# Kernel tuning notes

Measured on AMD Instinct MI355X. Metric: run time of the kernel, lower is better.

The kernel has to match this reference:

```python
import jax, jax.numpy as jnp
import numpy as np

# Hyperparameters from __init__
TEMPERATURE = 0.07
HARD_POS_W = 1.5
HARD_NEG_W = 2.0
THR_POS = 0.5
THR_NEG = 0.3
NEG_LOSS_W = 0.3

B, D, N_CLASSES = 8192, 256, 1024


def setup_inputs() -> dict:
    key = jax.random.key(0)
    kf, kl = jax.random.split(key)
    features = jax.random.normal(kf, (B, D), dtype=jnp.float32)
    labels = jax.random.randint(kl, (B,), 0, N_CLASSES, dtype=jnp.int32)
    return {"features": features, "labels": labels}


def reference(features, labels):
    b = features.shape[0]
    # L2-normalize features (F.normalize(dim=1))
    anchor = features / jnp.linalg.norm(features, axis=1, keepdims=True)
    sim = anchor @ anchor.T                      # [B, B] cosine similarity
    logits = sim / TEMPERATURE
    logits = logits - jax.lax.stop_gradient(jnp.max(logits, axis=1, keepdims=True))

    mask = (labels[:, None] == labels[None, :]).astype(logits.dtype)   # same-class
    logits_mask = 1.0 - jnp.eye(b, dtype=logits.dtype)                 # exclude self

    # W2ML weights: computed from detached similarities (torch used .item())
    sim_d = jax.lax.stop_gradient(sim)
    offdiag = logits_mask > 0
    is_pos = mask > 0
    hard_pos = is_pos & (sim_d < THR_POS) & offdiag
    pos_weights = jnp.where(
        hard_pos, 1.0 + (THR_POS - sim_d) / THR_POS * (HARD_POS_W - 1.0), 1.0)
    hard_neg = (~is_pos) & (sim_d > THR_NEG) & offdiag
    neg_weights = jnp.where(
        hard_neg, 1.0 + (sim_d - THR_NEG) / (1.0 - THR_NEG) * (HARD_NEG_W - 1.0), 1.0)

    # SupCon log-prob with self excluded from the denominator
    exp_logits = jnp.exp(logits) * logits_mask
    denom = jnp.sum(exp_logits, axis=1, keepdims=True)
    log_prob = logits - jnp.log(denom)

    pos_mask = mask * logits_mask
    pos_cnt = jnp.clip(jnp.sum(pos_mask, axis=1), 1.0, None)
    positive_loss = -jnp.mean(
        jnp.sum(pos_mask * pos_weights * log_prob, axis=1) / pos_cnt)

    # Negative term: weighted mean probability mass assigned to negatives
    neg_mask = (1.0 - mask) * logits_mask
    neg_cnt = jnp.clip(jnp.sum(neg_mask, axis=1), 1.0, None)
    prob = exp_logits / denom
    negative_loss = jnp.mean(
        jnp.sum(neg_mask * neg_weights * prob, axis=1) / neg_cnt)

    return positive_loss + NEG_LOSS_W * negative_loss
```

## Files before the change

kernel.cpp:

```cpp
#include <hip/hip_runtime.h>

#define BSZ  8192
#define DDIM 256
#define BM 128
#define BN 128
#define NT   64
#define NTRI (NT * (NT + 1) / 2)

typedef float f32x4 __attribute__((ext_vector_type(4)));
typedef short bf16x8 __attribute__((ext_vector_type(8)));

__device__ __forceinline__ unsigned short f32_to_bf16(float f) {
    unsigned int u = __float_as_uint(f);
    u += 0x7fffu + ((u >> 16) & 1u);
    return (unsigned short)(u >> 16);
}

#if __has_builtin(__builtin_amdgcn_exp2f)
__device__ __forceinline__ float fast_exp2(float x) { return __builtin_amdgcn_exp2f(x); }
#else
__device__ __forceinline__ float fast_exp2(float x) {
    float r;
    asm("v_exp_f32 %0, %1" : "=v"(r) : "v"(x));
    return r;
}
#endif

#define K_E1   20.60992915555662f
#define K_E2  -20.60992915555662f
#define K_INVT 14.285714285714286f
#define K_N1   1.4285714285714286f
#define K_N2   0.5714285714285714f

template<int CTRL>
__device__ __forceinline__ float dpp_add(float v) {
    int t = __builtin_amdgcn_update_dpp(0, __float_as_int(v), CTRL, 0xF, 0xF, true);
    return v + __int_as_float(t);
}
__device__ __forceinline__ float red16(float v) {
    v = dpp_add<0xB1>(v);
    v = dpp_add<0x4E>(v);
    v = dpp_add<0x141>(v);
    v = dpp_add<0x140>(v);
    return v;
}

__device__ __forceinline__ int swz(int b) {
    return b ^ ((((b >> 7) ^ (b >> 10)) & 7) << 4);
}

__device__ __forceinline__ void decode_tile(int t, int& It, int& Jt) {
    const int off1 = 136, off2 = 392, off3 = 648, off4 = 904, off5 = 1040,
              off6 = 1296, off7 = 1552, off8 = 1688, off9 = 1944;
    int b = (t >= off1) + (t >= off2) + (t >= off3) + (t >= off4) + (t >= off5)
          + (t >= off6) + (t >= off7) + (t >= off8) + (t >= off9);
    int si, sj, r0;
    switch (b) {
        case 0: si = 0; sj = 0; r0 = 0;    break;
        case 1: si = 0; sj = 1; r0 = off1; break;
        case 2: si = 0; sj = 2; r0 = off2; break;
        case 3: si = 0; sj = 3; r0 = off3; break;
        case 4: si = 1; sj = 1; r0 = off4; break;
        case 5: si = 1; sj = 2; r0 = off5; break;
        case 6: si = 1; sj = 3; r0 = off6; break;
        case 7: si = 2; sj = 2; r0 = off7; break;
        case 8: si = 2; sj = 3; r0 = off8; break;
        default: si = 3; sj = 3; r0 = off9; break;
    }
    const int rr = t - r0;
    int il, jl;
    if (si == sj) {
        il = 0;
        #pragma unroll
        for (int q = 1; q < 16; q++) if (rr >= (16 * q - (q * (q - 1)) / 2)) il = q;
        jl = il + (rr - (16 * il - (il * (il - 1)) / 2));
    } else {
        il = rr >> 4;
        jl = rr & 15;
    }
    It = si * 16 + il;
    Jt = sj * 16 + jl;
}

__global__ __launch_bounds__(256) void norm_kernel(const float* __restrict__ feat,
                                                   unsigned short* __restrict__ anchorT,
                                                   float* __restrict__ posAcc,
                                                   unsigned int* __restrict__ counter) {
    __shared__ __align__(16) unsigned short img[8 * 512];
    char* const imgb = (char*)img;
    const int tid  = threadIdx.x;
    const int wid  = tid >> 6;
    const int lane = tid & 63;
    const int R    = blockIdx.x;
    const int R0   = R * 16;

    if (tid < 64) posAcc[blockIdx.x * 64 + tid] = 0.0f;
    if (blockIdx.x == 0 && tid == 0) *counter = 0u;

    #pragma unroll
    for (int it = 0; it < 4; it++) {
        const int row = R0 + it * 4 + wid;
        const float4 v = ((const float4*)(feat + (size_t)row * DDIM))[lane];
        float ss = v.x * v.x + v.y * v.y + v.z * v.z + v.w * v.w;
        #pragma unroll
        for (int off = 32; off > 0; off >>= 1) ss += __shfl_xor(ss, off, 64);
        const float inv = rsqrtf(ss);
        ushort4 o;
        o.x = f32_to_bf16(v.x * inv);
        o.y = f32_to_bf16(v.y * inv);
        o.z = f32_to_bf16(v.z * inv);
        o.w = f32_to_bf16(v.w * inv);
        const int C    = lane >> 3;
        const int l16  = (row & 15) + (((lane >> 1) & 3) << 4);
        const int wb   = (C << 10) + (l16 << 4) + ((lane & 1) << 3);
        *(ushort4*)(imgb + swz(wb)) = o;
    }
    __syncthreads();
    #pragma unroll
    for (int p = 0; p < 2; p++) {
        const int c = p * 4 + wid;
        *(bf16x8*)(anchorT + ((size_t)(c * 512 + R)) * 512 + lane * 8) =
            *(const bf16x8*)(imgb + swz((c << 10) + (lane << 4)));
    }
}

__device__ __forceinline__ void gload_lds16(const unsigned short* g, unsigned short* l) {
    __builtin_amdgcn_global_load_lds(
        (const __attribute__((address_space(1))) void*)g,
        (__attribute__((address_space(3))) void*)l, 16, 0, 0);
}

__global__ __launch_bounds__(512) void simloss_kernel(
    const unsigned short* __restrict__ anchorT,
    const int* __restrict__ labels,
    float* __restrict__ part,
    float* __restrict__ posAcc)
{
    __shared__ __align__(16) unsigned short As[8 * 512];
    __shared__ __align__(16) unsigned short As2[8 * 512];
    __shared__ __align__(16) unsigned short Bs[8 * 512];
    __shared__ __align__(16) unsigned short Bs2[8 * 512];
    __shared__ float rowDT[2][BM][2];
    __shared__ float colDT[4][BN][2];
    __shared__ int rowLab[BM];
    __shared__ int colLab[BN];

    int It, Jt;
    decode_tile(blockIdx.x, It, Jt);
    const bool diag = (It == Jt);
    const int I0 = It * BM, J0 = Jt * BN;

    const int tid  = threadIdx.x;
    const int lane = tid & 63;
    const int w    = tid >> 6;
    const int rw   = w >> 1;
    const int cw   = w & 1;
    const int cl   = lane & 15;
    const int rg   = lane >> 4;
    const int laneOff = lane * 8;

    if (tid < BM) rowLab[tid] = labels[I0 + tid];
    else if (tid < 2 * BM) colLab[tid - BM] = labels[J0 + tid - BM];

    f32x4 acc[2][4];
    #pragma unroll
    for (int f = 0; f < 2; f++)
        #pragma unroll
        for (int g = 0; g < 4; g++)
            acc[f][g] = (f32x4){0.f, 0.f, 0.f, 0.f};

    const unsigned short* aSrc = anchorT + (size_t)It * 4096 + tid * 8;
    const unsigned short* bSrc = anchorT + (size_t)Jt * 4096 + tid * 8;
    unsigned short* const aD0 = &As[w * 512];
    unsigned short* const aD1 = &As2[w * 512];
    unsigned short* const bD0 = &Bs[w * 512];
    unsigned short* const bD1 = &Bs2[w * 512];

    gload_lds16(aSrc, aD0);
    gload_lds16(bSrc, bD0);

    #pragma unroll
    for (int c = 0; c < 8; c++) {
        if (c < 7) {
            const size_t off = (size_t)(c + 1) * 262144;
            gload_lds16(aSrc + off, ((c + 1) & 1) ? aD1 : aD0);
            gload_lds16(bSrc + off, ((c + 1) & 1) ? bD1 : bD0);
            asm volatile("s_waitcnt vmcnt(2)" ::: "memory");
        } else {
            asm volatile("s_waitcnt vmcnt(0)" ::: "memory");
        }
        __builtin_amdgcn_s_barrier();
        __builtin_amdgcn_sched_barrier(0);

        const unsigned short* aB = ((c & 1) ? As2 : As) + (rw * 2) * 512 + laneOff;
        const unsigned short* bB = ((c & 1) ? Bs2 : Bs) + (cw * 4) * 512 + laneOff;
        const bf16x8 a0 = *(const bf16x8*)(aB);
        const bf16x8 a1 = *(const bf16x8*)(aB + 512);
        const bf16x8 b0 = *(const bf16x8*)(bB);
        const bf16x8 b1 = *(const bf16x8*)(bB + 512);
        const bf16x8 b2 = *(const bf16x8*)(bB + 1024);
        const bf16x8 b3 = *(const bf16x8*)(bB + 1536);
        acc[0][0] = __builtin_amdgcn_mfma_f32_16x16x32_bf16(a0, b0, acc[0][0], 0, 0, 0);
        acc[0][1] = __builtin_amdgcn_mfma_f32_16x16x32_bf16(a0, b1, acc[0][1], 0, 0, 0);
        acc[0][2] = __builtin_amdgcn_mfma_f32_16x16x32_bf16(a0, b2, acc[0][2], 0, 0, 0);
        acc[0][3] = __builtin_amdgcn_mfma_f32_16x16x32_bf16(a0, b3, acc[0][3], 0, 0, 0);
        acc[1][0] = __builtin_amdgcn_mfma_f32_16x16x32_bf16(a1, b0, acc[1][0], 0, 0, 0);
        acc[1][1] = __builtin_amdgcn_mfma_f32_16x16x32_bf16(a1, b1, acc[1][1], 0, 0, 0);
        acc[1][2] = __builtin_amdgcn_mfma_f32_16x16x32_bf16(a1, b2, acc[1][2], 0, 0, 0);
        acc[1][3] = __builtin_amdgcn_mfma_f32_16x16x32_bf16(a1, b3, acc[1][3], 0, 0, 0);

        if (c < 7) {
            asm volatile("s_waitcnt lgkmcnt(0)" ::: "memory");
            __builtin_amdgcn_s_barrier();
        }
    }

    int ljr[4], gjr[4];
    #pragma unroll
    for (int g = 0; g < 4; g++) {
        const int cidx = cw * 64 + g * 16 + cl;
        ljr[g] = colLab[cidx];
        gjr[g] = J0 + cidx;
    }
    float cd[4] = {0.f, 0.f, 0.f, 0.f}, ct[4] = {0.f, 0.f, 0.f, 0.f};

    #pragma unroll
    for (int f = 0; f < 2; f++) {
        float rd[4] = {0.f, 0.f, 0.f, 0.f}, rt[4] = {0.f, 0.f, 0.f, 0.f};
        int li[4], gi[4];
        #pragma unroll
        for (int r = 0; r < 4; r++) {
            const int ridx = rw * 32 + f * 16 + rg * 4 + r;
            li[r] = rowLab[ridx];
            gi[r] = I0 + ridx;
        }
        #pragma unroll
        for (int g = 0; g < 4; g++) {
            const int lj = ljr[g];
            const bool granule = (rw * 2 + f) == (cw * 4 + g);
            const f32x4 c = acc[f][g];
            #pragma unroll
            for (int r = 0; r < 4; r++) {
                const float s = c[r];
                const bool self = diag && granule && ((rg * 4 + r) == cl);
                const float e  = self ? 0.f : fast_exp2(fmaf(s, K_E1, K_E2));
                const float wn = fmaxf(fmaf(s, K_N1, K_N2), 1.0f);
                const float we = wn * e;
                rd[r] += e;  rt[r] += we;
                if (!diag) { cd[g] += e; ct[g] += we; }
                if (li[r] == lj && !self) {
                    const float wp = fmaxf(1.5f - s, 1.0f);
                    const float slp = fmaf(s, K_INVT, -K_INVT) * wp;
                    float* pi = posAcc + (size_t)gi[r] * 4;
                    atomicAdd(pi + 0, slp);
                    atomicAdd(pi + 1, wp);
                    atomicAdd(pi + 2, we);
                    atomicAdd(pi + 3, 1.0f);
                    if (!diag) {
                        float* pj = posAcc + (size_t)gjr[g] * 4;
                        atomicAdd(pj + 0, slp);
                        atomicAdd(pj + 1, wp);
                        atomicAdd(pj + 2, we);
                        atomicAdd(pj + 3, 1.0f);
                    }
                }
            }
        }
        #pragma unroll
        for (int r = 0; r < 4; r++) {
            rd[r] = red16(rd[r]);
            rt[r] = red16(rt[r]);
        }
        if (cl == 0) {
            #pragma unroll
            for (int r = 0; r < 4; r++) {
                const int row = rw * 32 + f * 16 + rg * 4 + r;
                rowDT[cw][row][0] = rd[r];
                rowDT[cw][row][1] = rt[r];
            }
        }
    }
    if (!diag) {
        #pragma unroll
        for (int g = 0; g < 4; g++) {
            cd[g] += __shfl_xor(cd[g], 16, 64);
            cd[g] += __shfl_xor(cd[g], 32, 64);
            ct[g] += __shfl_xor(ct[g], 16, 64);
            ct[g] += __shfl_xor(ct[g], 32, 64);
        }
        if (rg == 0) {
            #pragma unroll
            for (int g = 0; g < 4; g++) {
                const int col = cw * 64 + g * 16 + cl;
                colDT[rw][col][0] = cd[g];
                colDT[rw][col][1] = ct[g];
            }
        }
    }

    __syncthreads();
    if (tid < BM) {
        float2 v;
        v.x = rowDT[0][tid][0] + rowDT[1][tid][0];
        v.y = rowDT[0][tid][1] + rowDT[1][tid][1];
        ((float2*)part)[(size_t)Jt * BSZ + I0 + tid] = v;
    } else if (tid < 2 * BM && !diag) {
        const int c = tid - BM;
        float2 v;
        v.x = colDT[0][c][0] + colDT[1][c][0] + colDT[2][c][0] + colDT[3][c][0];
        v.y = colDT[0][c][1] + colDT[1][c][1] + colDT[2][c][1] + colDT[3][c][1];
        ((float2*)part)[(size_t)It * BSZ + J0 + c] = v;
    }
}

__global__ __launch_bounds__(256) void reduce_final_kernel(
    const float* __restrict__ part, const float* __restrict__ posAcc,
    double* __restrict__ partial, unsigned int* __restrict__ counter,
    float* __restrict__ out)
{
    const int t   = threadIdx.x;
    const int row = blockIdx.x * 32 + (t >> 3);
    const int sg  = t & 7;
    float dsum = 0.f, T2 = 0.f;
    const float2* p2 = (const float2*)part;
    #pragma unroll
    for (int j = 0; j < 8; j++) {
        const float2 v = p2[(size_t)(sg * 8 + j) * BSZ + row];
        dsum += v.x; T2 += v.y;
    }
    #pragma unroll
    for (int off = 1; off < 8; off <<= 1) {
        dsum += __shfl_xor(dsum, off, 64);
        T2   += __shfl_xor(T2,   off, 64);
    }
    __shared__ double sp[32], sn[32];
    if (sg == 0) {
        const float4 pa = ((const float4*)posAcc)[row];
        const float s1 = pa.x, w1 = pa.y, s2 = T2 - pa.z, cnt = pa.w;
        const float pc = fmaxf(cnt, 1.0f);
        const float nc = fmaxf(8191.0f - cnt, 1.0f);
        const float ld = logf(dsum);
        sp[t >> 3] = (double)((s1 - ld * w1) / pc);
        sn[t >> 3] = (double)((s2 / dsum) / nc);
    }
    __syncthreads();
    __shared__ bool amLast;
    if (t < 32) {
        double p = sp[t], n = sn[t];
        #pragma unroll
        for (int off = 1; off < 32; off <<= 1) {
            p += __shfl_xor(p, off, 64);
            n += __shfl_xor(n, off, 64);
        }
        if (t == 0) {
            partial[blockIdx.x * 2 + 0] = p;
            partial[blockIdx.x * 2 + 1] = n;
            __threadfence();
            amLast = (atomicAdd(counter, 1u) == 255u);
        }
    }
    __syncthreads();
    if (amLast) {
        __threadfence();
        __shared__ double fp[256], fn[256];
        volatile double* vp = (volatile double*)partial;
        fp[t] = vp[t * 2 + 0];
        fn[t] = vp[t * 2 + 1];
        __syncthreads();
        for (int s = 128; s > 0; s >>= 1) {
            if (t < s) { fp[t] += fp[t + s]; fn[t] += fn[t + s]; }
            __syncthreads();
        }
        if (t == 0) out[0] = (float)(-fp[0] / (double)BSZ + 0.3 * (fn[0] / (double)BSZ));
    }
}

extern "C" void kernel_launch(void* const* d_in, const int* in_sizes, int n_in,
                              void* d_out, int out_size, void* d_ws, size_t ws_size,
                              hipStream_t stream) {
    const float* feat = (const float*)d_in[0];
    const int* labels = (const int*)d_in[1];
    float* out = (float*)d_out;

    char* ws = (char*)d_ws;
    unsigned short* anchorT = (unsigned short*)ws;
    const size_t anchorBytes = (size_t)BSZ * DDIM * sizeof(unsigned short);
    float* part = (float*)(ws + anchorBytes);
    const size_t partBytes = (size_t)NT * BSZ * 2 * sizeof(float);
    float* posAcc = (float*)(ws + anchorBytes + partBytes);
    const size_t posBytes = (size_t)BSZ * 4 * sizeof(float);
    double* partial = (double*)(ws + anchorBytes + partBytes + posBytes);
    unsigned int* counter = (unsigned int*)(ws + anchorBytes + partBytes + posBytes + 4096);

    norm_kernel<<<BSZ / 16, 256, 0, stream>>>(feat, anchorT, posAcc, counter);
    simloss_kernel<<<NTRI, 512, 0, stream>>>(anchorT, labels, part, posAcc);
    reduce_final_kernel<<<BSZ / 32, 256, 0, stream>>>(part, posAcc, partial, counter, out);
}
```

Measured before the change: 109.5 us.

## Skip hard-negative weighting when no tile similarity exceeds threshold, alias LDS scratch

The epilogue now computes the hard-negative weighted sum only when a wave-wide max of similarities exceeds the threshold. Otherwise the weighted total equals the plain exp sum, so the per-element weight arithmetic is skipped; when it is needed, exp is recomputed in a second pass. Label lookups move from LDS staging to direct global loads, and the row/col reduction buffers alias the operand LDS tiles. This cuts LDS use, allowing a launch bound of 8 waves per SIMD and so more occupancy, but the tighter bound may cap registers and cause spills.

```diff
diff --git a/kernel.cpp b/kernel.cpp
--- a/kernel.cpp
+++ b/kernel.cpp
@@ -130,7 +130,7 @@
         (__attribute__((address_space(3))) void*)l, 16, 0, 0);
 }
 
-__global__ __launch_bounds__(512) void simloss_kernel(
+__global__ __launch_bounds__(512, 8) void simloss_kernel(
     const unsigned short* __restrict__ anchorT,
     const int* __restrict__ labels,
     float* __restrict__ part,
@@ -140,10 +140,8 @@
     __shared__ __align__(16) unsigned short As2[8 * 512];
     __shared__ __align__(16) unsigned short Bs[8 * 512];
     __shared__ __align__(16) unsigned short Bs2[8 * 512];
-    __shared__ float rowDT[2][BM][2];
-    __shared__ float colDT[4][BN][2];
-    __shared__ int rowLab[BM];
-    __shared__ int colLab[BN];
+    float* const rowDT = (float*)As;
+    float* const colDT = (float*)Bs;
 
     int It, Jt;
     decode_tile(blockIdx.x, It, Jt);
@@ -158,9 +156,6 @@
     const int cl   = lane & 15;
     const int rg   = lane >> 4;
     const int laneOff = lane * 8;
-
-    if (tid < BM) rowLab[tid] = labels[I0 + tid];
-    else if (tid < 2 * BM) colLab[tid - BM] = labels[J0 + tid - BM];
 
     f32x4 acc[2][4];
     #pragma unroll
@@ -215,28 +210,33 @@
         }
     }
 
-    int ljr[4], gjr[4];
-    #pragma unroll
-    for (int g = 0; g < 4; g++) {
-        const int cidx = cw * 64 + g * 16 + cl;
-        ljr[g] = colLab[cidx];
-        gjr[g] = J0 + cidx;
-    }
-    float cd[4] = {0.f, 0.f, 0.f, 0.f}, ct[4] = {0.f, 0.f, 0.f, 0.f};
+    int lj[4];
+    #pragma unroll
+    for (int g = 0; g < 4; g++) lj[g] = labels[J0 + cw * 64 + g * 16 + cl];
+
+    float m8[8];
+    #pragma unroll
+    for (int f = 0; f < 2; f++)
+        #pragma unroll
+        for (int g = 0; g < 4; g++) {
+            const f32x4 c = acc[f][g];
+            m8[f * 4 + g] = fmaxf(fmaxf(c[0], c[1]), fmaxf(c[2], c[3]));
+        }
+    const float mx = fmaxf(fmaxf(fmaxf(m8[0], m8[1]), fmaxf(m8[2], m8[3])),
+                           fmaxf(fmaxf(m8[4], m8[5]), fmaxf(m8[6], m8[7])));
+    const bool needW = __any(fmaf(mx, K_N1, K_N2) > 1.0f) != 0;
+
+    float cd[4] = {0.f, 0.f, 0.f, 0.f};
 
     #pragma unroll
     for (int f = 0; f < 2; f++) {
-        float rd[4] = {0.f, 0.f, 0.f, 0.f}, rt[4] = {0.f, 0.f, 0.f, 0.f};
-        int li[4], gi[4];
-        #pragma unroll
-        for (int r = 0; r < 4; r++) {
-            const int ridx = rw * 32 + f * 16 + rg * 4 + r;
-            li[r] = rowLab[ridx];
-            gi[r] = I0 + ridx;
-        }
+        float rd[4] = {0.f, 0.f, 0.f, 0.f};
+        const int rbase = I0 + rw * 32 + f * 16 + rg * 4;
+        const int4 lv = *(const int4*)(labels + rbase);
+        const int li[4] = {lv.x, lv.y, lv.z, lv.w};
         #pragma unroll
         for (int g = 0; g < 4; g++) {
-            const int lj = ljr[g];
+            const int lj_ = lj[g];
             const bool granule = (rw * 2 + f) == (cw * 4 + g);
             const f32x4 c = acc[f][g];
             #pragma unroll
@@ -244,20 +244,20 @@
                 const float s = c[r];
                 const bool self = diag && granule && ((rg * 4 + r) == cl);
                 const float e  = self ? 0.f : fast_exp2(fmaf(s, K_E1, K_E2));
-                const float wn = fmaxf(fmaf(s, K_N1, K_N2), 1.0f);
-                const float we = wn * e;
-                rd[r] += e;  rt[r] += we;
-                if (!diag) { cd[g] += e; ct[g] += we; }
-                if (li[r] == lj && !self) {
+                rd[r] += e;
+                if (!diag) cd[g] += e;
+                if (li[r] == lj_ && !self) {
+                    const float wn = fmaxf(fmaf(s, K_N1, K_N2), 1.0f);
+                    const float we = wn * e;
                     const float wp = fmaxf(1.5f - s, 1.0f);
                     const float slp = fmaf(s, K_INVT, -K_INVT) * wp;
-                    float* pi = posAcc + (size_t)gi[r] * 4;
+                    float* pi = posAcc + (size_t)(rbase + r) * 4;
                     atomicAdd(pi + 0, slp);
                     atomicAdd(pi + 1, wp);
                     atomicAdd(pi + 2, we);
                     atomicAdd(pi + 3, 1.0f);
                     if (!diag) {
-                        float* pj = posAcc + (size_t)gjr[g] * 4;
+                        float* pj = posAcc + (size_t)(J0 + cw * 64 + g * 16 + cl) * 4;
                         atomicAdd(pj + 0, slp);
                         atomicAdd(pj + 1, wp);
                         atomicAdd(pj + 2, we);
@@ -266,6 +266,27 @@
                 }
             }
         }
+        float rt[4];
+        if (!needW) {
+            #pragma unroll
+            for (int r = 0; r < 4; r++) rt[r] = rd[r];
+        } else {
+            #pragma unroll
+            for (int r = 0; r < 4; r++) rt[r] = 0.f;
+            #pragma unroll
+            for (int g = 0; g < 4; g++) {
+                const bool granule = (rw * 2 + f) == (cw * 4 + g);
+                const f32x4 c = acc[f][g];
+                #pragma unroll
+                for (int r = 0; r < 4; r++) {
+                    const float s = c[r];
+                    const bool self = diag && granule && ((rg * 4 + r) == cl);
+                    const float e  = self ? 0.f : fast_exp2(fmaf(s, K_E1, K_E2));
+                    const float wn = fmaxf(fmaf(s, K_N1, K_N2), 1.0f);
+                    rt[r] += wn * e;
+                }
+            }
+        }
         #pragma unroll
         for (int r = 0; r < 4; r++) {
             rd[r] = red16(rd[r]);
@@ -275,12 +296,34 @@
             #pragma unroll
             for (int r = 0; r < 4; r++) {
                 const int row = rw * 32 + f * 16 + rg * 4 + r;
-                rowDT[cw][row][0] = rd[r];
-                rowDT[cw][row][1] = rt[r];
+                rowDT[(cw * BM + row) * 2 + 0] = rd[r];
+                rowDT[(cw * BM + row) * 2 + 1] = rt[r];
             }
         }
     }
+
     if (!diag) {
+        float ct[4];
+        if (!needW) {
+            #pragma unroll
+            for (int g = 0; g < 4; g++) ct[g] = cd[g];
+        } else {
+            #pragma unroll
+            for (int g = 0; g < 4; g++) ct[g] = 0.f;
+            #pragma unroll
+            for (int f = 0; f < 2; f++)
+                #pragma unroll
+                for (int g = 0; g < 4; g++) {
+                    const f32x4 c = acc[f][g];
+                    #pragma unroll
+                    for (int r = 0; r < 4; r++) {
+                        const float s = c[r];
+                        const float e  = fast_exp2(fmaf(s, K_E1, K_E2));
+                        const float wn = fmaxf(fmaf(s, K_N1, K_N2), 1.0f);
+                        ct[g] += wn * e;
+                    }
+                }
+        }
         #pragma unroll
         for (int g = 0; g < 4; g++) {
             cd[g] += __shfl_xor(cd[g], 16, 64);
@@ -292,8 +335,8 @@
             #pragma unroll
             for (int g = 0; g < 4; g++) {
                 const int col = cw * 64 + g * 16 + cl;
-                colDT[rw][col][0] = cd[g];
-                colDT[rw][col][1] = ct[g];
+                colDT[(rw * BN + col) * 2 + 0] = cd[g];
+                colDT[(rw * BN + col) * 2 + 1] = ct[g];
             }
         }
     }
@@ -301,14 +344,16 @@
     __syncthreads();
     if (tid < BM) {
         float2 v;
-        v.x = rowDT[0][tid][0] + rowDT[1][tid][0];
-        v.y = rowDT[0][tid][1] + rowDT[1][tid][1];
+        v.x = rowDT[(0 * BM + tid) * 2 + 0] + rowDT[(1 * BM + tid) * 2 + 0];
+        v.y = rowDT[(0 * BM + tid) * 2 + 1] + rowDT[(1 * BM + tid) * 2 + 1];
         ((float2*)part)[(size_t)Jt * BSZ + I0 + tid] = v;
     } else if (tid < 2 * BM && !diag) {
         const int c = tid - BM;
         float2 v;
-        v.x = colDT[0][c][0] + colDT[1][c][0] + colDT[2][c][0] + colDT[3][c][0];
-        v.y = colDT[0][c][1] + colDT[1][c][1] + colDT[2][c][1] + colDT[3][c][1];
+        v.x = colDT[(0 * BN + c) * 2 + 0] + colDT[(1 * BN + c) * 2 + 0]
+            + colDT[(2 * BN + c) * 2 + 0] + colDT[(3 * BN + c) * 2 + 0];
+        v.y = colDT[(0 * BN + c) * 2 + 1] + colDT[(1 * BN + c) * 2 + 1]
+            + colDT[(2 * BN + c) * 2 + 1] + colDT[(3 * BN + c) * 2 + 1];
         ((float2*)part)[(size_t)It * BSZ + J0 + c] = v;
     }
 }
```

After: 194.4 us. 77.6% more time.

## Use 4-wave blocks covering full tile width per wave and drop LDS staging

Applied to the files above, without the earlier changes.

Each block now runs 256 threads (4 waves) instead of 512, and each wave computes a 32x128 slab with 16 accumulator tiles instead of 32x64, so every wave reuses its A fragments across all 8 column groups. Each thread issues twice as many global-to-LDS loads per stage. Row labels are read straight from global memory, and row partial sums are written directly to global memory, which removes the rowDT and label LDS arrays and the cross-wave row reduction. The column reduction reuses the A buffer as scratch. Launch bounds target 3 blocks per CU, trading more registers per wave and fewer waves per block for less LDS traffic and less synchronization.

```diff
diff --git a/kernel.cpp b/kernel.cpp
--- a/kernel.cpp
+++ b/kernel.cpp
@@ -130,20 +130,17 @@
         (__attribute__((address_space(3))) void*)l, 16, 0, 0);
 }
 
-__global__ __launch_bounds__(512) void simloss_kernel(
+__global__ __launch_bounds__(256, 3) void simloss_kernel(
     const unsigned short* __restrict__ anchorT,
     const int* __restrict__ labels,
     float* __restrict__ part,
     float* __restrict__ posAcc)
 {
-    __shared__ __align__(16) unsigned short As[8 * 512];
+    __shared__ __align__(16) unsigned short As [8 * 512];
     __shared__ __align__(16) unsigned short As2[8 * 512];
-    __shared__ __align__(16) unsigned short Bs[8 * 512];
+    __shared__ __align__(16) unsigned short Bs [8 * 512];
     __shared__ __align__(16) unsigned short Bs2[8 * 512];
-    __shared__ float rowDT[2][BM][2];
-    __shared__ float colDT[4][BN][2];
-    __shared__ int rowLab[BM];
-    __shared__ int colLab[BN];
+    float* const colDT = (float*)As;
 
     int It, Jt;
     decode_tile(blockIdx.x, It, Jt);
@@ -153,111 +150,108 @@
     const int tid  = threadIdx.x;
     const int lane = tid & 63;
     const int w    = tid >> 6;
-    const int rw   = w >> 1;
-    const int cw   = w & 1;
     const int cl   = lane & 15;
     const int rg   = lane >> 4;
     const int laneOff = lane * 8;
 
-    if (tid < BM) rowLab[tid] = labels[I0 + tid];
-    else if (tid < 2 * BM) colLab[tid - BM] = labels[J0 + tid - BM];
-
-    f32x4 acc[2][4];
+    f32x4 acc[2][8];
     #pragma unroll
     for (int f = 0; f < 2; f++)
         #pragma unroll
-        for (int g = 0; g < 4; g++)
+        for (int g = 0; g < 8; g++)
             acc[f][g] = (f32x4){0.f, 0.f, 0.f, 0.f};
 
-    const unsigned short* aSrc = anchorT + (size_t)It * 4096 + tid * 8;
-    const unsigned short* bSrc = anchorT + (size_t)Jt * 4096 + tid * 8;
-    unsigned short* const aD0 = &As[w * 512];
-    unsigned short* const aD1 = &As2[w * 512];
-    unsigned short* const bD0 = &Bs[w * 512];
-    unsigned short* const bD1 = &Bs2[w * 512];
-
-    gload_lds16(aSrc, aD0);
-    gload_lds16(bSrc, bD0);
+    const unsigned short* aSrc = anchorT + (size_t)It * 4096;
+    const unsigned short* bSrc = anchorT + (size_t)Jt * 4096;
+
+    #define STAGE(c, Ad, Bd)                                                   \
+        do {                                                                   \
+            const size_t off = (size_t)(c) * 262144;                           \
+            gload_lds16(aSrc + off + tid * 8,        (Ad) + w * 512);          \
+            gload_lds16(aSrc + off + 2048 + tid * 8, (Ad) + 2048 + w * 512);   \
+            gload_lds16(bSrc + off + tid * 8,        (Bd) + w * 512);          \
+            gload_lds16(bSrc + off + 2048 + tid * 8, (Bd) + 2048 + w * 512);   \
+        } while (0)
+
+    STAGE(0, As, Bs);
 
     #pragma unroll
     for (int c = 0; c < 8; c++) {
         if (c < 7) {
-            const size_t off = (size_t)(c + 1) * 262144;
-            gload_lds16(aSrc + off, ((c + 1) & 1) ? aD1 : aD0);
-            gload_lds16(bSrc + off, ((c + 1) & 1) ? bD1 : bD0);
-            asm volatile("s_waitcnt vmcnt(2)" ::: "memory");
+            if ((c + 1) & 1) STAGE(c + 1, As2, Bs2);
+            else             STAGE(c + 1, As,  Bs);
+            asm volatile("s_waitcnt vmcnt(4)" ::: "memory");
         } else {
             asm volatile("s_waitcnt vmcnt(0)" ::: "memory");
         }
         __builtin_amdgcn_s_barrier();
         __builtin_amdgcn_sched_barrier(0);
 
-        const unsigned short* aB = ((c & 1) ? As2 : As) + (rw * 2) * 512 + laneOff;
-        const unsigned short* bB = ((c & 1) ? Bs2 : Bs) + (cw * 4) * 512 + laneOff;
+        const unsigned short* aB = ((c & 1) ? As2 : As) + (w * 2) * 512 + laneOff;
+        const unsigned short* bB = ((c & 1) ? Bs2 : Bs) + laneOff;
         const bf16x8 a0 = *(const bf16x8*)(aB);
         const bf16x8 a1 = *(const bf16x8*)(aB + 512);
-        const bf16x8 b0 = *(const bf16x8*)(bB);
-        const bf16x8 b1 = *(const bf16x8*)(bB + 512);
-        const bf16x8 b2 = *(const bf16x8*)(bB + 1024);
-        const bf16x8 b3 = *(const bf16x8*)(bB + 1536);
-        acc[0][0] = __builtin_amdgcn_mfma_f32_16x16x32_bf16(a0, b0, acc[0][0], 0, 0, 0);
-        acc[0][1] = __builtin_amdgcn_mfma_f32_16x16x32_bf16(a0, b1, acc[0][1], 0, 0, 0);
-        acc[0][2] = __builtin_amdgcn_mfma_f32_16x16x32_bf16(a0, b2, acc[0][2], 0, 0, 0);
-        acc[0][3] = __builtin_amdgcn_mfma_f32_16x16x32_bf16(a0, b3, acc[0][3], 0, 0, 0);
-        acc[1][0] = __builtin_amdgcn_mfma_f32_16x16x32_bf16(a1, b0, acc[1][0], 0, 0, 0);
-        acc[1][1] = __builtin_amdgcn_mfma_f32_16x16x32_bf16(a1, b1, acc[1][1], 0, 0, 0);
-        acc[1][2] = __builtin_amdgcn_mfma_f32_16x16x32_bf16(a1, b2, acc[1][2], 0, 0, 0);
-        acc[1][3] = __builtin_amdgcn_mfma_f32_16x16x32_bf16(a1, b3, acc[1][3], 0, 0, 0);
+        #pragma unroll
+        for (int gh = 0; gh < 2; gh++) {
+            const bf16x8 b0 = *(const bf16x8*)(bB + (gh * 4 + 0) * 512);
+            const bf16x8 b1 = *(const bf16x8*)(bB + (gh * 4 + 1) * 512);
+            const bf16x8 b2 = *(const bf16x8*)(bB + (gh * 4 + 2) * 512);
+            const bf16x8 b3 = *(const bf16x8*)(bB + (gh * 4 + 3) * 512);
+            acc[0][gh*4+0] = __builtin_amdgcn_mfma_f32_16x16x32_bf16(a0, b0, acc[0][gh*4+0], 0, 0, 0);
+            acc[1][gh*4+0] = __builtin_amdgcn_mfma_f32_16x16x32_bf16(a1, b0, acc[1][gh*4+0], 0, 0, 0);
+            acc[0][gh*4+1] = __builtin_amdgcn_mfma_f32_16x16x32_bf16(a0, b1, acc[0][gh*4+1], 0, 0, 0);
+            acc[1][gh*4+1] = __builtin_amdgcn_mfma_f32_16x16x32_bf16(a1, b1, acc[1][gh*4+1], 0, 0, 0);
+            acc[0][gh*4+2] = __builtin_amdgcn_mfma_f32_16x16x32_bf16(a0, b2, acc[0][gh*4+2], 0, 0, 0);
+            acc[1][gh*4+2] = __builtin_amdgcn_mfma_f32_16x16x32_bf16(a1, b2, acc[1][gh*4+2], 0, 0, 0);
+            acc[0][gh*4+3] = __builtin_amdgcn_mfma_f32_16x16x32_bf16(a0, b3, acc[0][gh*4+3], 0, 0, 0);
+            acc[1][gh*4+3] = __builtin_amdgcn_mfma_f32_16x16x32_bf16(a1, b3, acc[1][gh*4+3], 0, 0, 0);
+        }
 
         if (c < 7) {
             asm volatile("s_waitcnt lgkmcnt(0)" ::: "memory");
             __builtin_amdgcn_s_barrier();
         }
     }
-
-    int ljr[4], gjr[4];
-    #pragma unroll
-    for (int g = 0; g < 4; g++) {
-        const int cidx = cw * 64 + g * 16 + cl;
-        ljr[g] = colLab[cidx];
-        gjr[g] = J0 + cidx;
-    }
-    float cd[4] = {0.f, 0.f, 0.f, 0.f}, ct[4] = {0.f, 0.f, 0.f, 0.f};
+    #undef STAGE
+
+    int lj[8];
+    #pragma unroll
+    for (int g = 0; g < 8; g++) lj[g] = labels[J0 + g * 16 + cl];
+
+    float cd[8] = {0.f,0.f,0.f,0.f,0.f,0.f,0.f,0.f};
+    float ct[8] = {0.f,0.f,0.f,0.f,0.f,0.f,0.f,0.f};
+    float2* const part2 = (float2*)part;
 
     #pragma unroll
     for (int f = 0; f < 2; f++) {
         float rd[4] = {0.f, 0.f, 0.f, 0.f}, rt[4] = {0.f, 0.f, 0.f, 0.f};
-        int li[4], gi[4];
-        #pragma unroll
-        for (int r = 0; r < 4; r++) {
-            const int ridx = rw * 32 + f * 16 + rg * 4 + r;
-            li[r] = rowLab[ridx];
-            gi[r] = I0 + ridx;
-        }
-        #pragma unroll
-        for (int g = 0; g < 4; g++) {
-            const int lj = ljr[g];
-            const bool granule = (rw * 2 + f) == (cw * 4 + g);
-            const f32x4 c = acc[f][g];
+        const int rbase = I0 + w * 32 + f * 16 + rg * 4;
+        const int4 lv = *(const int4*)(labels + rbase);
+        const int li[4] = {lv.x, lv.y, lv.z, lv.w};
+        #pragma unroll
+        for (int g = 0; g < 8; g++) {
+            const int lj_ = lj[g];
+            const bool granule = (w * 2 + f) == g;
+            const f32x4 c4 = acc[f][g];
             #pragma unroll
             for (int r = 0; r < 4; r++) {
-                const float s = c[r];
+                const float s = c4[r];
                 const bool self = diag && granule && ((rg * 4 + r) == cl);
                 const float e  = self ? 0.f : fast_exp2(fmaf(s, K_E1, K_E2));
                 const float wn = fmaxf(fmaf(s, K_N1, K_N2), 1.0f);
                 const float we = wn * e;
                 rd[r] += e;  rt[r] += we;
                 if (!diag) { cd[g] += e; ct[g] += we; }
-                if (li[r] == lj && !self) {
+                if (li[r] == lj_ && !self) {
                     const float wp = fmaxf(1.5f - s, 1.0f);
                     const float slp = fmaf(s, K_INVT, -K_INVT) * wp;
-                    float* pi = posAcc + (size_t)gi[r] * 4;
+                    float* pi = posAcc + (size_t)(rbase + r) * 4;
                     atomicAdd(pi + 0, slp);
                     atomicAdd(pi + 1, wp);
                     atomicAdd(pi + 2, we);
                     atomicAdd(pi + 3, 1.0f);
                     if (!diag) {
-                        float* pj = posAcc + (size_t)gjr[g] * 4;
+                        float* pj = posAcc + (size_t)(J0 + g * 16 + cl) * 4;
                         atomicAdd(pj + 0, slp);
                         atomicAdd(pj + 1, wp);
                         atomicAdd(pj + 2, we);
@@ -274,15 +268,15 @@
         if (cl == 0) {
             #pragma unroll
             for (int r = 0; r < 4; r++) {
-                const int row = rw * 32 + f * 16 + rg * 4 + r;
-                rowDT[cw][row][0] = rd[r];
-                rowDT[cw][row][1] = rt[r];
+                float2 v; v.x = rd[r]; v.y = rt[r];
+                part2[(size_t)Jt * BSZ + rbase + r] = v;
             }
         }
     }
+
     if (!diag) {
         #pragma unroll
-        for (int g = 0; g < 4; g++) {
+        for (int g = 0; g < 8; g++) {
             cd[g] += __shfl_xor(cd[g], 16, 64);
             cd[g] += __shfl_xor(cd[g], 32, 64);
             ct[g] += __shfl_xor(ct[g], 16, 64);
@@ -290,26 +284,23 @@
         }
         if (rg == 0) {
             #pragma unroll
-            for (int g = 0; g < 4; g++) {
-                const int col = cw * 64 + g * 16 + cl;
-                colDT[rw][col][0] = cd[g];
-                colDT[rw][col][1] = ct[g];
+            for (int g = 0; g < 8; g++) {
+                const int col = g * 16 + cl;
+                colDT[(w * BN + col) * 2 + 0] = cd[g];
+                colDT[(w * BN + col) * 2 + 1] = ct[g];
             }
         }
     }
 
     __syncthreads();
-    if (tid < BM) {
+    if (tid >= 128 && !diag) {
+        const int col = tid - 128;
         float2 v;
-        v.x = rowDT[0][tid][0] + rowDT[1][tid][0];
-        v.y = rowDT[0][tid][1] + rowDT[1][tid][1];
-        ((float2*)part)[(size_t)Jt * BSZ + I0 + tid] = v;
-    } else if (tid < 2 * BM && !diag) {
-        const int c = tid - BM;
-        float2 v;
-        v.x = colDT[0][c][0] + colDT[1][c][0] + colDT[2][c][0] + colDT[3][c][0];
-        v.y = colDT[0][c][1] + colDT[1][c][1] + colDT[2][c][1] + colDT[3][c][1];
-        ((float2*)part)[(size_t)It * BSZ + J0 + c] = v;
+        v.x = colDT[(0 * BN + col) * 2 + 0] + colDT[(1 * BN + col) * 2 + 0]
+            + colDT[(2 * BN + col) * 2 + 0] + colDT[(3 * BN + col) * 2 + 0];
+        v.y = colDT[(0 * BN + col) * 2 + 1] + colDT[(1 * BN + col) * 2 + 1]
+            + colDT[(2 * BN + col) * 2 + 1] + colDT[(3 * BN + col) * 2 + 1];
+        part2[(size_t)It * BSZ + J0 + col] = v;
     }
 }
 
@@ -393,6 +384,6 @@
     unsigned int* counter = (unsigned int*)(ws + anchorBytes + partBytes + posBytes + 4096);
 
     norm_kernel<<<BSZ / 16, 256, 0, stream>>>(feat, anchorT, posAcc, counter);
-    simloss_kernel<<<NTRI, 512, 0, stream>>>(anchorT, labels, part, posAcc);
+    simloss_kernel<<<NTRI, 256, 0, stream>>>(anchorT, labels, part, posAcc);
     reduce_final_kernel<<<BSZ / 32, 256, 0, stream>>>(part, posAcc, partial, counter, out);
 }
```

New measurement: 110.1 us. No clear change (+0.6%).
